# Kernel tuning notes

Measured on AMD Instinct MI355X. Metric: run time of the kernel, lower is better.

## Reference

```python
import jax, jax.numpy as jnp
import numpy as np

TEMPERATURE = 0.5
EPS = 1e-12  # matches torch F.normalize default eps


def setup_inputs() -> dict:
    key = jax.random.key(0)
    k1, k2 = jax.random.split(key)
    proj_1 = jax.random.normal(k1, (4096, 128), dtype=jnp.float32)
    proj_2 = jax.random.normal(k2, (4096, 128), dtype=jnp.float32)
    return {"proj_1": proj_1, "proj_2": proj_2}


def _l2_normalize(x):
    # torch F.normalize(p=2): x / max(||x||, eps)
    norm = jnp.linalg.norm(x, axis=1, keepdims=True)
    return x / jnp.maximum(norm, EPS)


def reference(proj_1, proj_2):
    n = proj_1.shape[0]
    z_i = _l2_normalize(proj_1)
    z_j = _l2_normalize(proj_2)
    reps = jnp.concatenate([z_i, z_j], axis=0)            # [2N, D]
    # cosine similarity of normalized vectors == dot product
    sim = reps @ reps.T                                    # [2N, 2N]
    sim_ij = jnp.diagonal(sim, offset=n)                   # [N]
    sim_ji = jnp.diagonal(sim, offset=-n)                  # [N]
    positives = jnp.concatenate([sim_ij, sim_ji], axis=0)  # [2N]
    nominator = jnp.exp(positives / TEMPERATURE)
    mask = 1.0 - jnp.eye(2 * n, dtype=sim.dtype)           # zero out self-similarity
    denominator = jnp.sum(mask * jnp.exp(sim / TEMPERATURE), axis=1)  # [2N]
    all_losses = -jnp.log(nominator / denominator)
    loss = jnp.sum(all_losses) / (2 * n)
    return loss
```

## Files before the change

### kernel.cpp

```cpp
#include <hip/hip_runtime.h>
#include <stdint.h>

typedef __bf16 bf16;
typedef bf16 bf16x8 __attribute__((ext_vector_type(8)));
typedef float floatx4 __attribute__((ext_vector_type(4)));

#define INV_T 2.0f

__global__ __launch_bounds__(256) void nrm_kernel(const float* __restrict__ p1,
                                                  const float* __restrict__ p2,
                                                  unsigned* __restrict__ reps) {
    int gt   = blockIdx.x * 256 + threadIdx.x;
    int row  = gt >> 6;
    int lane = gt & 63;
    const float* srcRow = (row < 4096) ? (p1 + (size_t)row * 128)
                                       : (p2 + (size_t)(row - 4096) * 128);
    float2 v = ((const float2*)srcRow)[lane];
    float ss = v.x * v.x + v.y * v.y;
#pragma unroll
    for (int s = 1; s < 64; s <<= 1) ss += __shfl_xor(ss, s, 64);
    float inv = 1.0f / fmaxf(sqrtf(ss), 1e-12f);
    union { bf16 h[2]; unsigned u; } pk;
    pk.h[0] = (bf16)(v.x * inv);
    pk.h[1] = (bf16)(v.y * inv);
    reps[(size_t)row * 64 + lane] = pk.u;
}

__global__ __launch_bounds__(256, 2) void sim_kernel(const bf16* __restrict__ reps,
                                                     float* __restrict__ rowsum,
                                                     float* __restrict__ pos) {
    __shared__ bf16 lA[128 * 128];
    __shared__ bf16 lB[128 * 128];

    const int cg   = blockIdx.x;
    const int bi   = blockIdx.y;
    const int tid  = threadIdx.x;
    const int w    = tid >> 6;
    const int lane = tid & 63;
    const int quad = lane >> 4;
    const int lcol = lane & 15;

    const int rowTileBase = bi * 128;

    {
        const uint4* gA = (const uint4*)(reps + (size_t)rowTileBase * 128);
        uint4* sA = (uint4*)lA;
#pragma unroll
        for (int i = 0; i < 8; i++) sA[i * 256 + tid] = gA[i * 256 + tid];
    }
    __syncthreads();

    const int wRow = (w >> 1) * 64;
    const int wCol = (w & 1) * 64;

    bf16x8 aF[4][4];
#pragma unroll
    for (int mi = 0; mi < 4; mi++)
#pragma unroll
        for (int ks = 0; ks < 4; ks++) {
            int r = wRow + mi * 16 + lcol;
            int k = ks * 32 + quad * 8;
            aF[mi][ks] = *(const bf16x8*)&lA[r * 128 + k];
        }

    float rs[16];
#pragma unroll
    for (int i = 0; i < 16; i++) rs[i] = 0.0f;

    for (int cj = 0; cj < 8; cj++) {
        const int colTileBase = cg * 1024 + cj * 128;
        __syncthreads();
        {
            const uint4* gB = (const uint4*)(reps + (size_t)colTileBase * 128);
            uint4* sB = (uint4*)lB;
#pragma unroll
            for (int i = 0; i < 8; i++) sB[i * 256 + tid] = gB[i * 256 + tid];
        }
        __syncthreads();

        floatx4 acc[4][4];
        const floatx4 zf = {0.0f, 0.0f, 0.0f, 0.0f};
#pragma unroll
        for (int mi = 0; mi < 4; mi++)
#pragma unroll
            for (int ni = 0; ni < 4; ni++) acc[mi][ni] = zf;

#pragma unroll
        for (int ks = 0; ks < 4; ks++) {
#pragma unroll
            for (int ni = 0; ni < 4; ni++) {
                int c = wCol + ni * 16 + lcol;
                int k = ks * 32 + quad * 8;
                bf16x8 bF = *(const bf16x8*)&lB[c * 128 + k];
#pragma unroll
                for (int mi = 0; mi < 4; mi++)
                    acc[mi][ni] = __builtin_amdgcn_mfma_f32_16x16x32_bf16(
                        aF[mi][ks], bF, acc[mi][ni], 0, 0, 0);
            }
        }

        const int rowB = rowTileBase + wRow;
        const int colB = colTileBase + wCol;
        const bool diagT = (colTileBase == rowTileBase);
        const bool partT = (colTileBase == ((rowTileBase + 4096) & 8191));
        if (diagT | partT) {
#pragma unroll
            for (int mi = 0; mi < 4; mi++)
#pragma unroll
                for (int ni = 0; ni < 4; ni++)
#pragma unroll
                    for (int r = 0; r < 4; r++) {
                        int grow = rowB + mi * 16 + quad * 4 + r;
                        int gcol = colB + ni * 16 + lcol;
                        float s = acc[mi][ni][r];
                        if (partT && gcol == ((grow + 4096) & 8191)) pos[grow] = s;
                        float e = __expf(s * INV_T);
                        if (diagT && grow == gcol) e = 0.0f;
                        rs[mi * 4 + r] += e;
                    }
        } else {
#pragma unroll
            for (int mi = 0; mi < 4; mi++)
#pragma unroll
                for (int ni = 0; ni < 4; ni++)
#pragma unroll
                    for (int r = 0; r < 4; r++)
                        rs[mi * 4 + r] += __expf(acc[mi][ni][r] * INV_T);
        }
    }

#pragma unroll
    for (int s = 1; s < 16; s <<= 1)
#pragma unroll
        for (int k = 0; k < 16; k++) rs[k] += __shfl_xor(rs[k], s, 64);

    if (lcol == 0) {
#pragma unroll
        for (int k = 0; k < 16; k++) {
            int grow = rowTileBase + wRow + (k >> 2) * 16 + quad * 4 + (k & 3);
            atomicAdd(&rowsum[grow], rs[k]);
        }
    }
}

__global__ __launch_bounds__(256) void fin_kernel(const float* __restrict__ rowsum,
                                                  const float* __restrict__ pos,
                                                  float* __restrict__ out) {
    int r = blockIdx.x * 256 + threadIdx.x;
    float v = logf(rowsum[r]) - pos[r] * INV_T;
#pragma unroll
    for (int s = 1; s < 64; s <<= 1) v += __shfl_xor(v, s, 64);
    __shared__ float red[4];
    if ((threadIdx.x & 63) == 0) red[threadIdx.x >> 6] = v;
    __syncthreads();
    if (threadIdx.x == 0) {
        float t = (red[0] + red[1]) + (red[2] + red[3]);
        atomicAdd(out, t * (1.0f / 8192.0f));
    }
}

extern "C" void kernel_launch(void* const* d_in, const int* in_sizes, int n_in,
                              void* d_out, int out_size, void* d_ws, size_t ws_size,
                              hipStream_t stream) {
    const float* p1 = (const float*)d_in[0];
    const float* p2 = (const float*)d_in[1];
    float* out = (float*)d_out;

    char* ws     = (char*)d_ws;
    bf16* reps   = (bf16*)ws;
    float* rowsum = (float*)(ws + (2u << 20));
    float* pos    = (float*)(ws + (2u << 20) + (32u << 10));

    hipMemsetAsync(rowsum, 0, 8192 * sizeof(float), stream);
    hipMemsetAsync(out, 0, sizeof(float), stream);

    nrm_kernel<<<2048, 256, 0, stream>>>(p1, p2, (unsigned*)reps);
    sim_kernel<<<dim3(8, 64), 256, 0, stream>>>(reps, rowsum, pos);
    fin_kernel<<<32, 256, 0, stream>>>(rowsum, pos, out);
}
```

Baseline: 95.00 us.

## Load MFMA operands directly from global, use exp2, drop atomics and memsets

The sim kernel no longer stages A and B tiles in LDS. Operands are read straight from global memory (L2/L1-cached), which removes the barriers and LDS traffic. The exponential is now computed with a native exp2 on a prescaled argument. Per-wave row sums go into 16 partial buffers instead of being added atomically, so the two memsets disappear. A single-block final kernel then reduces the partials and writes the loss directly. The trade-offs are heavy repeated global loads with uncoalesced 16-byte row accesses for B, and a serial one-block finish.

```diff
diff --git a/kernel.cpp b/kernel.cpp
--- a/kernel.cpp
+++ b/kernel.cpp
@@ -6,6 +6,7 @@
 typedef float floatx4 __attribute__((ext_vector_type(4)));
 
 #define INV_T 2.0f
+#define EXP2_SCALE 2.8853900817779268f
 
 __global__ __launch_bounds__(256) void nrm_kernel(const float* __restrict__ p1,
                                                   const float* __restrict__ p2,
@@ -27,11 +28,8 @@
 }
 
 __global__ __launch_bounds__(256, 2) void sim_kernel(const bf16* __restrict__ reps,
-                                                     float* __restrict__ rowsum,
+                                                     float* __restrict__ rowsum16,
                                                      float* __restrict__ pos) {
-    __shared__ bf16 lA[128 * 128];
-    __shared__ bf16 lB[128 * 128];
-
     const int cg   = blockIdx.x;
     const int bi   = blockIdx.y;
     const int tid  = threadIdx.x;
@@ -41,15 +39,6 @@
     const int lcol = lane & 15;
 
     const int rowTileBase = bi * 128;
-
-    {
-        const uint4* gA = (const uint4*)(reps + (size_t)rowTileBase * 128);
-        uint4* sA = (uint4*)lA;
-#pragma unroll
-        for (int i = 0; i < 8; i++) sA[i * 256 + tid] = gA[i * 256 + tid];
-    }
-    __syncthreads();
-
     const int wRow = (w >> 1) * 64;
     const int wCol = (w & 1) * 64;
 
@@ -58,9 +47,9 @@
     for (int mi = 0; mi < 4; mi++)
 #pragma unroll
         for (int ks = 0; ks < 4; ks++) {
-            int r = wRow + mi * 16 + lcol;
+            int r = rowTileBase + wRow + mi * 16 + lcol;
             int k = ks * 32 + quad * 8;
-            aF[mi][ks] = *(const bf16x8*)&lA[r * 128 + k];
+            aF[mi][ks] = *(const bf16x8*)(reps + (size_t)r * 128 + k);
         }
 
     float rs[16];
@@ -69,14 +58,6 @@
 
     for (int cj = 0; cj < 8; cj++) {
         const int colTileBase = cg * 1024 + cj * 128;
-        __syncthreads();
-        {
-            const uint4* gB = (const uint4*)(reps + (size_t)colTileBase * 128);
-            uint4* sB = (uint4*)lB;
-#pragma unroll
-            for (int i = 0; i < 8; i++) sB[i * 256 + tid] = gB[i * 256 + tid];
-        }
-        __syncthreads();
 
         floatx4 acc[4][4];
         const floatx4 zf = {0.0f, 0.0f, 0.0f, 0.0f};
@@ -86,17 +67,19 @@
             for (int ni = 0; ni < 4; ni++) acc[mi][ni] = zf;
 
 #pragma unroll
-        for (int ks = 0; ks < 4; ks++) {
+        for (int ni = 0; ni < 4; ni++) {
+            const int c = colTileBase + wCol + ni * 16 + lcol;
+            const bf16* bRow = reps + (size_t)c * 128;
+            bf16x8 bF[4];
 #pragma unroll
-            for (int ni = 0; ni < 4; ni++) {
-                int c = wCol + ni * 16 + lcol;
-                int k = ks * 32 + quad * 8;
-                bf16x8 bF = *(const bf16x8*)&lB[c * 128 + k];
+            for (int ks = 0; ks < 4; ks++)
+                bF[ks] = *(const bf16x8*)(bRow + ks * 32 + quad * 8);
+#pragma unroll
+            for (int ks = 0; ks < 4; ks++)
 #pragma unroll
                 for (int mi = 0; mi < 4; mi++)
                     acc[mi][ni] = __builtin_amdgcn_mfma_f32_16x16x32_bf16(
-                        aF[mi][ks], bF, acc[mi][ni], 0, 0, 0);
-            }
+                        aF[mi][ks], bF[ks], acc[mi][ni], 0, 0, 0);
         }
 
         const int rowB = rowTileBase + wRow;
@@ -114,7 +97,7 @@
                         int gcol = colB + ni * 16 + lcol;
                         float s = acc[mi][ni][r];
                         if (partT && gcol == ((grow + 4096) & 8191)) pos[grow] = s;
-                        float e = __expf(s * INV_T);
+                        float e = __builtin_amdgcn_exp2f(s * EXP2_SCALE);
                         if (diagT && grow == gcol) e = 0.0f;
                         rs[mi * 4 + r] += e;
                     }
@@ -125,7 +108,7 @@
                 for (int ni = 0; ni < 4; ni++)
 #pragma unroll
                     for (int r = 0; r < 4; r++)
-                        rs[mi * 4 + r] += __expf(acc[mi][ni][r] * INV_T);
+                        rs[mi * 4 + r] += __builtin_amdgcn_exp2f(acc[mi][ni][r] * EXP2_SCALE);
         }
     }
 
@@ -135,27 +118,37 @@
         for (int k = 0; k < 16; k++) rs[k] += __shfl_xor(rs[k], s, 64);
 
     if (lcol == 0) {
+        float* dst = rowsum16 + (size_t)(cg * 2 + (w & 1)) * 8192;
 #pragma unroll
         for (int k = 0; k < 16; k++) {
             int grow = rowTileBase + wRow + (k >> 2) * 16 + quad * 4 + (k & 3);
-            atomicAdd(&rowsum[grow], rs[k]);
+            dst[grow] = rs[k];
         }
     }
 }
 
-__global__ __launch_bounds__(256) void fin_kernel(const float* __restrict__ rowsum,
-                                                  const float* __restrict__ pos,
-                                                  float* __restrict__ out) {
-    int r = blockIdx.x * 256 + threadIdx.x;
-    float v = logf(rowsum[r]) - pos[r] * INV_T;
+__global__ __launch_bounds__(1024) void fin_kernel(const float* __restrict__ rowsum16,
+                                                   const float* __restrict__ pos,
+                                                   float* __restrict__ out) {
+    float v = 0.0f;
+#pragma unroll
+    for (int rr = 0; rr < 8; rr++) {
+        int r = rr * 1024 + threadIdx.x;
+        float d = 0.0f;
+#pragma unroll
+        for (int p = 0; p < 16; p++) d += rowsum16[p * 8192 + r];
+        v += logf(d) - pos[r] * INV_T;
+    }
 #pragma unroll
     for (int s = 1; s < 64; s <<= 1) v += __shfl_xor(v, s, 64);
-    __shared__ float red[4];
+    __shared__ float red[16];
     if ((threadIdx.x & 63) == 0) red[threadIdx.x >> 6] = v;
     __syncthreads();
     if (threadIdx.x == 0) {
-        float t = (red[0] + red[1]) + (red[2] + red[3]);
-        atomicAdd(out, t * (1.0f / 8192.0f));
+        float t = 0.0f;
+#pragma unroll
+        for (int i = 0; i < 16; i++) t += red[i];
+        *out = t * (1.0f / 8192.0f);
     }
 }
 
@@ -166,15 +159,12 @@
     const float* p2 = (const float*)d_in[1];
     float* out = (float*)d_out;
 
-    char* ws     = (char*)d_ws;
-    bf16* reps   = (bf16*)ws;
-    float* rowsum = (float*)(ws + (2u << 20));
-    float* pos    = (float*)(ws + (2u << 20) + (32u << 10));
-
-    hipMemsetAsync(rowsum, 0, 8192 * sizeof(float), stream);
-    hipMemsetAsync(out, 0, sizeof(float), stream);
+    char* ws       = (char*)d_ws;
+    bf16* reps     = (bf16*)ws;
+    float* rowsum16 = (float*)(ws + (2u << 20));
+    float* pos      = (float*)(ws + (2u << 20) + (512u << 10));
 
     nrm_kernel<<<2048, 256, 0, stream>>>(p1, p2, (unsigned*)reps);
-    sim_kernel<<<dim3(8, 64), 256, 0, stream>>>(reps, rowsum, pos);
-    fin_kernel<<<32, 256, 0, stream>>>(rowsum, pos, out);
+    sim_kernel<<<dim3(8, 64), 256, 0, stream>>>(reps, rowsum16, pos);
+    fin_kernel<<<1, 1024, 0, stream>>>(rowsum16, pos, out);
 }
```

After: 126.5 us. +33.1%, slower.
